# Kernel optimization log

Hardware: AMD Instinct MI355X
Metric: run time of the kernel (lower is better)

The kernel has to match this reference:

```python
import jax, jax.numpy as jnp
import numpy as np

N = 50000
NEG_SLOPE = 0.2  # PyG GATConv default negative_slope


def _gat_layer(x, src, dst, edge_attr, W, We, a_src, a_dst, a_edge, bias):
    """Single-head PyG GATConv (heads=1, concat=True, add_self_loops=True,
    fill_value='mean' for self-loop edge_attr, dropout inactive / eval mode)."""
    n = x.shape[0]
    # add self loops; self-loop edge_attr = per-feature mean of edge_attr
    loop = jnp.arange(n)
    src2 = jnp.concatenate([src, loop])
    dst2 = jnp.concatenate([dst, loop])
    ea_loop = jnp.broadcast_to(edge_attr.mean(axis=0, keepdims=True), (n, edge_attr.shape[1]))
    ea = jnp.concatenate([edge_attr, ea_loop], axis=0)          # [E', edge_dim]

    h = x @ W                                                    # [N, C_out]
    a_s = h @ a_src                                              # [N]
    a_d = h @ a_dst                                              # [N]
    a_e = (ea @ We) @ a_edge                                     # [E']

    alpha = jax.nn.leaky_relu(a_s[src2] + a_d[dst2] + a_e, NEG_SLOPE)  # [E']
    # segment softmax over incoming edges of each dst node
    amax = jax.ops.segment_max(alpha, dst2, num_segments=n)     # [N]
    ex = jnp.exp(alpha - amax[dst2])                             # [E']
    denom = jax.ops.segment_sum(ex, dst2, num_segments=n)       # [N]
    w = ex / denom[dst2]                                         # [E']

    msg = h[src2] * w[:, None]                                   # [E', C_out]
    out = jax.ops.segment_sum(msg, dst2, num_segments=n) + bias  # [N, C_out]
    return out


def setup_inputs() -> dict:
    key = jax.random.key(0)
    ks = jax.random.split(key, 16)
    E, C_in, C_h, C_out, Ed = 800000, 128, 256, 128, 8
    s = 0.05
    inp = {
        "x": jax.random.normal(ks[0], (N, C_in), dtype=jnp.float32),
        "edge_index": jax.random.randint(ks[1], (2, E), 0, N, dtype=jnp.int32),
        "edge_attr": jax.random.normal(ks[2], (E, Ed), dtype=jnp.float32),
        # layer 1 params
        "W1": jax.random.normal(ks[3], (C_in, C_h), dtype=jnp.float32) * s,
        "We1": jax.random.normal(ks[4], (Ed, C_h), dtype=jnp.float32) * s,
        "as1": jax.random.normal(ks[5], (C_h,), dtype=jnp.float32) * s,
        "ad1": jax.random.normal(ks[6], (C_h,), dtype=jnp.float32) * s,
        "ae1": jax.random.normal(ks[7], (C_h,), dtype=jnp.float32) * s,
        "b1": jnp.zeros((C_h,), dtype=jnp.float32),
        # layer 2 params
        "W2": jax.random.normal(ks[8], (C_h, C_out), dtype=jnp.float32) * s,
        "We2": jax.random.normal(ks[9], (Ed, C_out), dtype=jnp.float32) * s,
        "as2": jax.random.normal(ks[10], (C_out,), dtype=jnp.float32) * s,
        "ad2": jax.random.normal(ks[11], (C_out,), dtype=jnp.float32) * s,
        "ae2": jax.random.normal(ks[12], (C_out,), dtype=jnp.float32) * s,
        "b2": jnp.zeros((C_out,), dtype=jnp.float32),
    }
    return inp


def reference(x, edge_index, edge_attr, W1, We1, as1, ad1, ae1, b1,
              W2, We2, as2, ad2, ae2, b2):
    src, dst = edge_index[0], edge_index[1]
    h = _gat_layer(x, src, dst, edge_attr, W1, We1, as1, ad1, ae1, b1)
    h = jax.nn.relu(h)  # relu between layers, not after last
    out = _gat_layer(h, src, dst, edge_attr, W2, We2, as2, ad2, ae2, b2)
    return out
```

## Files before the change

kernel.cpp:

```cpp
#include <hip/hip_runtime.h>
#include <hip/hip_bf16.h>


#define NEG_SLOPE 0.2f
#define EHB 1024

typedef unsigned short u16;
typedef short short8 __attribute__((ext_vector_type(8)));
typedef float v4f __attribute__((ext_vector_type(4)));
typedef u16 u16x4 __attribute__((ext_vector_type(4)));
typedef u16 u16x8 __attribute__((ext_vector_type(8)));

__device__ __forceinline__ u16 f2bf(float f) {
    unsigned u = __float_as_uint(f);
    return (u16)((u + 0x7fffu + ((u >> 16) & 1u)) >> 16);
}
__device__ __forceinline__ float bf2f(u16 h) {
    return __uint_as_float(((unsigned)h) << 16);
}
__device__ __forceinline__ float bf_lo(int v) { return __uint_as_float(((unsigned)v) << 16); }
__device__ __forceinline__ float bf_hi(int v) { return __uint_as_float(((unsigned)v) & 0xffff0000u); }
__device__ __forceinline__ float lrelu(float x) {
    return x >= 0.f ? x : NEG_SLOPE * x;
}
__device__ __forceinline__ int ld_acq(int* p) {
    return __hip_atomic_load(p, __ATOMIC_ACQUIRE, __HIP_MEMORY_SCOPE_AGENT);
}
__device__ __forceinline__ void st_rel(int* p, int v) {
    __hip_atomic_store(p, v, __ATOMIC_RELEASE, __HIP_MEMORY_SCOPE_AGENT);
}

__global__ __launch_bounds__(256) void pre_fat_kernel(
        const float* __restrict__ ea, const int* __restrict__ dst,
        const float* __restrict__ We1, const float* __restrict__ ae1v,
        const float* __restrict__ We2, const float* __restrict__ ae2v,
        float* __restrict__ mean_acc, int* __restrict__ deg,
        float2* __restrict__ aEe, int E,
        const float* __restrict__ W1, u16* __restrict__ w1thi, u16* __restrict__ w1tlo,
        const float* __restrict__ W2, u16* __restrict__ w2thi, u16* __restrict__ w2tlo,
        float* __restrict__ we_vec1g, float* __restrict__ we_vec2g) {
    int tid = threadIdx.x;
    if (blockIdx.x >= EHB) {
        int t = (blockIdx.x - EHB) * 256 + tid;
        if (t < 128 * 256) {
            int k = t >> 8, m = t & 255;
            float v = W1[t];
            u16 h = f2bf(v);
            w1thi[(size_t)m * 128 + k] = h;
            w1tlo[(size_t)m * 128 + k] = f2bf(v - bf2f(h));
        } else {
            t -= 128 * 256;
            int k = t >> 7, m = t & 127;
            float v = W2[t];
            u16 h = f2bf(v);
            w2thi[(size_t)m * 256 + k] = h;
            w2tlo[(size_t)m * 256 + k] = f2bf(v - bf2f(h));
        }
        return;
    }
    __shared__ float red[8];
    __shared__ float wv[16];
    if (tid < 16) { wv[tid] = 0.f; if (tid < 8) red[tid] = 0.f; }
    __syncthreads();
    {
        float a1 = ae1v[tid];
        int lane = tid & 63;
#pragma unroll
        for (int j = 0; j < 8; ++j) {
            float v = We1[j * 256 + tid] * a1;
#pragma unroll
            for (int o = 32; o; o >>= 1) v += __shfl_down(v, o);
            if (lane == 0) atomicAdd(&wv[j], v);
        }
        if (tid < 128) {
            float a2 = ae2v[tid];
#pragma unroll
            for (int j = 0; j < 8; ++j) {
                float v = We2[j * 128 + tid] * a2;
#pragma unroll
                for (int o = 32; o; o >>= 1) v += __shfl_down(v, o);
                if (lane == 0) atomicAdd(&wv[8 + j], v);
            }
        }
    }
    __syncthreads();
    if (blockIdx.x == 0 && tid < 16) {
        if (tid < 8) we_vec1g[tid] = wv[tid];
        else         we_vec2g[tid - 8] = wv[tid];
    }
    float s[8] = {0.f};
    int stride = EHB * 256;
    for (int e = blockIdx.x * 256 + tid; e < E; e += stride) {
        atomicAdd(&deg[dst[e]], 1);
        const float4 v0 = *(const float4*)&ea[(size_t)e * 8];
        const float4 v1 = *(const float4*)&ea[(size_t)e * 8 + 4];
        s[0] += v0.x; s[1] += v0.y; s[2] += v0.z; s[3] += v0.w;
        s[4] += v1.x; s[5] += v1.y; s[6] += v1.z; s[7] += v1.w;
        float s1 = v0.x * wv[0] + v0.y * wv[1] + v0.z * wv[2] + v0.w * wv[3]
                 + v1.x * wv[4] + v1.y * wv[5] + v1.z * wv[6] + v1.w * wv[7];
        float s2 = v0.x * wv[8] + v0.y * wv[9] + v0.z * wv[10] + v0.w * wv[11]
                 + v1.x * wv[12] + v1.y * wv[13] + v1.z * wv[14] + v1.w * wv[15];
        aEe[e] = make_float2(s1, s2);
    }
#pragma unroll
    for (int j = 0; j < 8; ++j) atomicAdd(&red[j], s[j]);
    __syncthreads();
    if (tid < 8) atomicAdd(&mean_acc[tid], red[tid]);
}

__global__ __launch_bounds__(256) void scan_fused_kernel(
        const int* __restrict__ deg, int* __restrict__ row_start,
        int* __restrict__ cursor, int* __restrict__ partials, int* __restrict__ pprefix,
        int* __restrict__ gcount, int* __restrict__ gflag, int N, int n,
        const float* __restrict__ mean_acc, float Einv,
        const float* __restrict__ we_vec1, const float* __restrict__ we_vec2,
        float* __restrict__ ae_loop) {
    __shared__ int s[256];
    __shared__ int amLast, bprefix;
    int t = threadIdx.x, bid = blockIdx.x;
    int i = bid * 256 + t;
    int v = (i < N) ? deg[i] : 0;
    s[t] = v; __syncthreads();
    for (int off = 1; off < 256; off <<= 1) {
        int u = (t >= off) ? s[t - off] : 0;
        __syncthreads();
        s[t] += u;
        __syncthreads();
    }
    int incl = s[t];
    int total = s[255];
    if (t == 0) {
        partials[bid] = total;
        __threadfence();
        int c = __hip_atomic_fetch_add(gcount, 1, __ATOMIC_ACQ_REL, __HIP_MEMORY_SCOPE_AGENT);
        amLast = (c == (int)gridDim.x - 1);
    }
    __syncthreads();
    if (amLast) {
        int G = gridDim.x;
        int pv = (t < G) ? ld_acq(&partials[t]) : 0;
        __syncthreads();
        s[t] = pv; __syncthreads();
        for (int off = 1; off < 256; off <<= 1) {
            int u = (t >= off) ? s[t - off] : 0;
            __syncthreads();
            s[t] += u;
            __syncthreads();
        }
        if (t < G) pprefix[t] = s[t] - pv;
        if (t == 0) {
            float s1 = 0.f, s2 = 0.f;
#pragma unroll
            for (int j = 0; j < 8; ++j) {
                float m = mean_acc[j] * Einv;
                s1 += m * we_vec1[j];
                s2 += m * we_vec2[j];
            }
            ae_loop[0] = s1; ae_loop[1] = s2;
        }
        __threadfence();
        __syncthreads();
        if (t == 0) st_rel(gflag, 1);
    }
    if (t == 0) {
        while (ld_acq(gflag) == 0) __builtin_amdgcn_s_sleep(2);
        bprefix = ld_acq(&pprefix[bid]);
    }
    __syncthreads();
    int ex = bprefix + incl - v;
    if (i < n) row_start[i] = ex;
    if (i < N) cursor[i] = ex;
}

#define BK 32
#define LDA 40
__global__ __launch_bounds__(256) void gemm1_fill_fat_kernel(
        const float* __restrict__ A32,
        const u16* __restrict__ Bh_g, const u16* __restrict__ Bl_g,
        u16* __restrict__ Cb, int Nrows, int K, int M,
        const float* __restrict__ av, const float* __restrict__ bv,
        float* __restrict__ as_out, float* __restrict__ ad_out, int Gg, int gx,
        const int* __restrict__ src, const int* __restrict__ dst,
        const float2* __restrict__ aEe, int* __restrict__ cursor,
        float4* __restrict__ epack, int E) {
    __shared__ u16 Ah[128 * LDA], Bh[128 * LDA], Bl[128 * LDA];
    int tid = threadIdx.x;
    if ((int)blockIdx.x >= Gg) {
        int e = ((int)blockIdx.x - Gg) * 256 + tid;
        if (e < E) {
            int d = dst[e];
            int idx = atomicAdd(&cursor[d], 1);
            float2 a = aEe[e];
            epack[idx] = make_float4(__int_as_float(src[e]), a.x, a.y, 0.f);
        }
        return;
    }
    int lane = tid & 63;
    int wv = tid >> 6;
    int wm = wv >> 1, wn = wv & 1;
    int l15 = lane & 15, quad = lane >> 4;
    int rb = ((int)blockIdx.x / gx) * 128;
    int cb = ((int)blockIdx.x % gx) * 128;

    v4f acc[4][4];
#pragma unroll
    for (int mi = 0; mi < 4; ++mi)
#pragma unroll
        for (int ni = 0; ni < 4; ++ni) acc[mi][ni] = (v4f){0.f, 0.f, 0.f, 0.f};

    int sr = tid >> 1;
    int sc = (tid & 1) * 16;

    for (int kc = 0; kc < K; kc += BK) {
        int gr = rb + sr;
        u16x8 a0 = {0,0,0,0,0,0,0,0}, a1 = {0,0,0,0,0,0,0,0};
        if (gr < Nrows) {
            const float* pa = A32 + (size_t)gr * K + kc + sc;
            float4 f0 = *(const float4*)pa;
            float4 f1 = *(const float4*)(pa + 4);
            float4 f2 = *(const float4*)(pa + 8);
            float4 f3 = *(const float4*)(pa + 12);
            a0 = (u16x8){f2bf(f0.x), f2bf(f0.y), f2bf(f0.z), f2bf(f0.w),
                         f2bf(f1.x), f2bf(f1.y), f2bf(f1.z), f2bf(f1.w)};
            a1 = (u16x8){f2bf(f2.x), f2bf(f2.y), f2bf(f2.z), f2bf(f2.w),
                         f2bf(f3.x), f2bf(f3.y), f2bf(f3.z), f2bf(f3.w)};
        }
        size_t bb = (size_t)(cb + sr) * K + kc + sc;
        u16x8 b0 = *(const u16x8*)(Bh_g + bb);
        u16x8 b1 = *(const u16x8*)(Bh_g + bb + 8);
        u16x8 b2 = *(const u16x8*)(Bl_g + bb);
        u16x8 b3 = *(const u16x8*)(Bl_g + bb + 8);
        *(u16x8*)&Ah[sr * LDA + sc] = a0;
        *(u16x8*)&Ah[sr * LDA + sc + 8] = a1;
        *(u16x8*)&Bh[sr * LDA + sc] = b0;
        *(u16x8*)&Bh[sr * LDA + sc + 8] = b1;
        *(u16x8*)&Bl[sr * LDA + sc] = b2;
        *(u16x8*)&Bl[sr * LDA + sc + 8] = b3;
        __syncthreads();
        short8 ah[4], bh[4], bl[4];
#pragma unroll
        for (int mi = 0; mi < 4; ++mi)
            ah[mi] = *(const short8*)&Ah[(wm * 64 + mi * 16 + l15) * LDA + quad * 8];
#pragma unroll
        for (int ni = 0; ni < 4; ++ni) {
            int r = (wn * 64 + ni * 16 + l15) * LDA + quad * 8;
            bh[ni] = *(const short8*)&Bh[r];
            bl[ni] = *(const short8*)&Bl[r];
        }
#pragma unroll
        for (int mi = 0; mi < 4; ++mi)
#pragma unroll
            for (int ni = 0; ni < 4; ++ni) {
                acc[mi][ni] = __builtin_amdgcn_mfma_f32_16x16x32_bf16(ah[mi], bh[ni], acc[mi][ni], 0, 0, 0);
                acc[mi][ni] = __builtin_amdgcn_mfma_f32_16x16x32_bf16(ah[mi], bl[ni], acc[mi][ni], 0, 0, 0);
            }
        __syncthreads();
    }
#pragma unroll
    for (int mi = 0; mi < 4; ++mi)
#pragma unroll
        for (int ni = 0; ni < 4; ++ni)
#pragma unroll
            for (int reg = 0; reg < 4; ++reg) {
                int row = rb + wm * 64 + mi * 16 + quad * 4 + reg;
                if (row < Nrows)
                    Cb[(size_t)row * M + cb + wn * 64 + ni * 16 + l15] = f2bf(acc[mi][ni][reg]);
            }
    float sd[4][4] = {}, dd[4][4] = {};
#pragma unroll
    for (int ni = 0; ni < 4; ++ni) {
        int col = cb + wn * 64 + ni * 16 + l15;
        float a = av[col], b = bv[col];
#pragma unroll
        for (int mi = 0; mi < 4; ++mi)
#pragma unroll
            for (int reg = 0; reg < 4; ++reg) {
                sd[mi][reg] += acc[mi][ni][reg] * a;
                dd[mi][reg] += acc[mi][ni][reg] * b;
            }
    }
#pragma unroll
    for (int off = 1; off < 16; off <<= 1)
#pragma unroll
        for (int mi = 0; mi < 4; ++mi)
#pragma unroll
            for (int reg = 0; reg < 4; ++reg) {
                sd[mi][reg] += __shfl_xor(sd[mi][reg], off);
                dd[mi][reg] += __shfl_xor(dd[mi][reg], off);
            }
    if (l15 == 0)
#pragma unroll
        for (int mi = 0; mi < 4; ++mi) {
            int row0 = rb + wm * 64 + mi * 16 + quad * 4;
#pragma unroll
            for (int reg = 0; reg < 4; ++reg)
                if (row0 + reg < Nrows) {
                    atomicAdd(as_out + row0 + reg, sd[mi][reg]);
                    atomicAdd(ad_out + row0 + reg, dd[mi][reg]);
                }
        }
}

__global__ __launch_bounds__(256) void gemm_mfma_kernel(
        const u16* __restrict__ A_g,
        const u16* __restrict__ Bh_g, const u16* __restrict__ Bl_g,
        u16* __restrict__ Cb, int Nrows, int K, int M,
        const float* __restrict__ av, const float* __restrict__ bv,
        float* __restrict__ as_out, float* __restrict__ ad_out) {
    __shared__ u16 Ah[128 * LDA], Bh[128 * LDA], Bl[128 * LDA];
    int tid = threadIdx.x;
    int lane = tid & 63;
    int wv = tid >> 6;
    int wm = wv >> 1, wn = wv & 1;
    int l15 = lane & 15, quad = lane >> 4;
    int rb = blockIdx.y * 128;
    int cb = blockIdx.x * 128;

    v4f acc[4][4];
#pragma unroll
    for (int mi = 0; mi < 4; ++mi)
#pragma unroll
        for (int ni = 0; ni < 4; ++ni) acc[mi][ni] = (v4f){0.f, 0.f, 0.f, 0.f};

    int sr = tid >> 1;
    int sc = (tid & 1) * 16;

    for (int kc = 0; kc < K; kc += BK) {
        int gr = rb + sr;
        u16x8 a0 = {0,0,0,0,0,0,0,0}, a1 = {0,0,0,0,0,0,0,0};
        if (gr < Nrows) {
            size_t ba = (size_t)gr * K + kc + sc;
            a0 = *(const u16x8*)(A_g + ba);
            a1 = *(const u16x8*)(A_g + ba + 8);
        }
        size_t bb = (size_t)(cb + sr) * K + kc + sc;
        u16x8 b0 = *(const u16x8*)(Bh_g + bb);
        u16x8 b1 = *(const u16x8*)(Bh_g + bb + 8);
        u16x8 b2 = *(const u16x8*)(Bl_g + bb);
        u16x8 b3 = *(const u16x8*)(Bl_g + bb + 8);
        *(u16x8*)&Ah[sr * LDA + sc] = a0;
        *(u16x8*)&Ah[sr * LDA + sc + 8] = a1;
        *(u16x8*)&Bh[sr * LDA + sc] = b0;
        *(u16x8*)&Bh[sr * LDA + sc + 8] = b1;
        *(u16x8*)&Bl[sr * LDA + sc] = b2;
        *(u16x8*)&Bl[sr * LDA + sc + 8] = b3;
        __syncthreads();
        short8 ah[4], bh[4], bl[4];
#pragma unroll
        for (int mi = 0; mi < 4; ++mi)
            ah[mi] = *(const short8*)&Ah[(wm * 64 + mi * 16 + l15) * LDA + quad * 8];
#pragma unroll
        for (int ni = 0; ni < 4; ++ni) {
            int r = (wn * 64 + ni * 16 + l15) * LDA + quad * 8;
            bh[ni] = *(const short8*)&Bh[r];
            bl[ni] = *(const short8*)&Bl[r];
        }
#pragma unroll
        for (int mi = 0; mi < 4; ++mi)
#pragma unroll
            for (int ni = 0; ni < 4; ++ni) {
                acc[mi][ni] = __builtin_amdgcn_mfma_f32_16x16x32_bf16(ah[mi], bh[ni], acc[mi][ni], 0, 0, 0);
                acc[mi][ni] = __builtin_amdgcn_mfma_f32_16x16x32_bf16(ah[mi], bl[ni], acc[mi][ni], 0, 0, 0);
            }
        __syncthreads();
    }
#pragma unroll
    for (int mi = 0; mi < 4; ++mi)
#pragma unroll
        for (int ni = 0; ni < 4; ++ni)
#pragma unroll
            for (int reg = 0; reg < 4; ++reg) {
                int row = rb + wm * 64 + mi * 16 + quad * 4 + reg;
                if (row < Nrows)
                    Cb[(size_t)row * M + cb + wn * 64 + ni * 16 + l15] = f2bf(acc[mi][ni][reg]);
            }
    float sd[4][4] = {}, dd[4][4] = {};
#pragma unroll
    for (int ni = 0; ni < 4; ++ni) {
        int col = cb + wn * 64 + ni * 16 + l15;
        float a = av[col], b = bv[col];
#pragma unroll
        for (int mi = 0; mi < 4; ++mi)
#pragma unroll
            for (int reg = 0; reg < 4; ++reg) {
                sd[mi][reg] += acc[mi][ni][reg] * a;
                dd[mi][reg] += acc[mi][ni][reg] * b;
            }
    }
#pragma unroll
    for (int off = 1; off < 16; off <<= 1)
#pragma unroll
        for (int mi = 0; mi < 4; ++mi)
#pragma unroll
            for (int reg = 0; reg < 4; ++reg) {
                sd[mi][reg] += __shfl_xor(sd[mi][reg], off);
                dd[mi][reg] += __shfl_xor(dd[mi][reg], off);
            }
    if (l15 == 0)
#pragma unroll
        for (int mi = 0; mi < 4; ++mi) {
            int row0 = rb + wm * 64 + mi * 16 + quad * 4;
#pragma unroll
            for (int reg = 0; reg < 4; ++reg)
                if (row0 + reg < Nrows) {
                    atomicAdd(as_out + row0 + reg, sd[mi][reg]);
                    atomicAdd(ad_out + row0 + reg, dd[mi][reg]);
                }
        }
}

__global__ __launch_bounds__(256) void agg1_kernel(const int* __restrict__ row_start,
                                                   const float4* __restrict__ epack,
                                                   const float* __restrict__ asv,
                                                   const float* __restrict__ adv,
                                                   const float* __restrict__ ae_loop,
                                                   const u16* __restrict__ Hb,
                                                   u16* __restrict__ ohi,
                                                   const float* __restrict__ bias, int N) {
    __shared__ float2 xch[4][64];
    int lane = threadIdx.x & 63;
    int wvi = threadIdx.x >> 6;
    int node = blockIdx.x * 4 + wvi;
    if (node >= N) return;
    int st = row_start[node], en = row_start[node + 1];
    float ad = adv[node];
    float aloop = lrelu(asv[node] + ad + ae_loop[0]);
    float m = aloop, sum = 1.f;
    float acc0, acc1, acc2, acc3;
    {
        int2 hv = *(const int2*)(Hb + (size_t)node * 256 + lane * 4);
        acc0 = bf_lo(hv.x); acc1 = bf_hi(hv.x);
        acc2 = bf_lo(hv.y); acc3 = bf_hi(hv.y);
    }
    for (int base = st; base < en; base += 64) {
        int i = base + lane;
        float al = -3.0e38f; int sreg = 0;
        if (i < en) {
            float4 ep = epack[i];
            sreg = __float_as_int(ep.x);
            al = lrelu(asv[sreg] + ad + ep.y);
        }
        float cm = al;
#pragma unroll
        for (int o = 1; o < 64; o <<= 1) cm = fmaxf(cm, __shfl_xor(cm, o));
        if (cm > m) {
            float sc = __expf(m - cm);
            acc0 *= sc; acc1 *= sc; acc2 *= sc; acc3 *= sc;
            sum *= sc; m = cm;
        }
        float w = (i < en) ? __expf(al - m) : 0.f;
        float wsum = w;
#pragma unroll
        for (int o = 1; o < 64; o <<= 1) wsum += __shfl_xor(wsum, o);
        sum += wsum;
        xch[wvi][lane] = make_float2(w, __int_as_float(sreg));
        int cnt = min(64, en - base);
        int j = 0;
        for (; j + 4 <= cnt; j += 4) {
            float2 e0 = xch[wvi][j], e1 = xch[wvi][j + 1];
            float2 e2 = xch[wvi][j + 2], e3 = xch[wvi][j + 3];
            int2 h0 = *(const int2*)(Hb + (size_t)__float_as_int(e0.y) * 256 + lane * 4);
            int2 h1 = *(const int2*)(Hb + (size_t)__float_as_int(e1.y) * 256 + lane * 4);
            int2 h2 = *(const int2*)(Hb + (size_t)__float_as_int(e2.y) * 256 + lane * 4);
            int2 h3 = *(const int2*)(Hb + (size_t)__float_as_int(e3.y) * 256 + lane * 4);
            acc0 += e0.x * bf_lo(h0.x) + e1.x * bf_lo(h1.x) + e2.x * bf_lo(h2.x) + e3.x * bf_lo(h3.x);
            acc1 += e0.x * bf_hi(h0.x) + e1.x * bf_hi(h1.x) + e2.x * bf_hi(h2.x) + e3.x * bf_hi(h3.x);
            acc2 += e0.x * bf_lo(h0.y) + e1.x * bf_lo(h1.y) + e2.x * bf_lo(h2.y) + e3.x * bf_lo(h3.y);
            acc3 += e0.x * bf_hi(h0.y) + e1.x * bf_hi(h1.y) + e2.x * bf_hi(h2.y) + e3.x * bf_hi(h3.y);
        }
        for (; j < cnt; ++j) {
            float2 e0 = xch[wvi][j];
            int2 h0 = *(const int2*)(Hb + (size_t)__float_as_int(e0.y) * 256 + lane * 4);
            acc0 += e0.x * bf_lo(h0.x); acc1 += e0.x * bf_hi(h0.x);
            acc2 += e0.x * bf_lo(h0.y); acc3 += e0.x * bf_hi(h0.y);
        }
    }
    float inv = 1.f / sum;
    const float4 bvv = *(const float4*)(bias + lane * 4);
    float t0 = acc0 * inv + bvv.x, t1 = acc1 * inv + bvv.y;
    float t2 = acc2 * inv + bvv.z, t3 = acc3 * inv + bvv.w;
    t0 = t0 > 0.f ? t0 : 0.f; t1 = t1 > 0.f ? t1 : 0.f;
    t2 = t2 > 0.f ? t2 : 0.f; t3 = t3 > 0.f ? t3 : 0.f;
    u16x4 h;
    h.x = f2bf(t0); h.y = f2bf(t1); h.z = f2bf(t2); h.w = f2bf(t3);
    *(u16x4*)(ohi + (size_t)node * 256 + lane * 4) = h;
}

__global__ __launch_bounds__(256) void agg2_kernel(const int* __restrict__ row_start,
                                                   const float4* __restrict__ epack,
                                                   const float* __restrict__ asv,
                                                   const float* __restrict__ adv,
                                                   const float* __restrict__ ae_loop,
                                                   const u16* __restrict__ Hb,
                                                   float* __restrict__ out,
                                                   const float* __restrict__ bias, int N) {
    __shared__ float2 xch[4][64];
    int lane = threadIdx.x & 63;
    int wvi = threadIdx.x >> 6;
    int node = blockIdx.x * 4 + wvi;
    if (node >= N) return;
    int st = row_start[node], en = row_start[node + 1];
    float ad = adv[node];
    float aloop = lrelu(asv[node] + ad + ae_loop[1]);
    float m = aloop, sum = 1.f;
    float acc0, acc1;
    {
        int hv = *(const int*)(Hb + (size_t)node * 128 + lane * 2);
        acc0 = bf_lo(hv); acc1 = bf_hi(hv);
    }
    for (int base = st; base < en; base += 64) {
        int i = base + lane;
        float al = -3.0e38f; int sreg = 0;
        if (i < en) {
            float4 ep = epack[i];
            sreg = __float_as_int(ep.x);
            al = lrelu(asv[sreg] + ad + ep.z);
        }
        float cm = al;
#pragma unroll
        for (int o = 1; o < 64; o <<= 1) cm = fmaxf(cm, __shfl_xor(cm, o));
        if (cm > m) {
            float sc = __expf(m - cm);
            acc0 *= sc; acc1 *= sc;
            sum *= sc; m = cm;
        }
        float w = (i < en) ? __expf(al - m) : 0.f;
        float wsum = w;
#pragma unroll
        for (int o = 1; o < 64; o <<= 1) wsum += __shfl_xor(wsum, o);
        sum += wsum;
        xch[wvi][lane] = make_float2(w, __int_as_float(sreg));
        int cnt = min(64, en - base);
        int j = 0;
        for (; j + 4 <= cnt; j += 4) {
            float2 e0 = xch[wvi][j], e1 = xch[wvi][j + 1];
            float2 e2 = xch[wvi][j + 2], e3 = xch[wvi][j + 3];
            int h0 = *(const int*)(Hb + (size_t)__float_as_int(e0.y) * 128 + lane * 2);
            int h1 = *(const int*)(Hb + (size_t)__float_as_int(e1.y) * 128 + lane * 2);
            int h2 = *(const int*)(Hb + (size_t)__float_as_int(e2.y) * 128 + lane * 2);
            int h3 = *(const int*)(Hb + (size_t)__float_as_int(e3.y) * 128 + lane * 2);
            acc0 += e0.x * bf_lo(h0) + e1.x * bf_lo(h1) + e2.x * bf_lo(h2) + e3.x * bf_lo(h3);
            acc1 += e0.x * bf_hi(h0) + e1.x * bf_hi(h1) + e2.x * bf_hi(h2) + e3.x * bf_hi(h3);
        }
        for (; j < cnt; ++j) {
            float2 e0 = xch[wvi][j];
            int h0 = *(const int*)(Hb + (size_t)__float_as_int(e0.y) * 128 + lane * 2);
            acc0 += e0.x * bf_lo(h0); acc1 += e0.x * bf_hi(h0);
        }
    }
    float inv = 1.f / sum;
    size_t o = (size_t)node * 128 + lane * 2;
    out[o]     = acc0 * inv + bias[lane * 2];
    out[o + 1] = acc1 * inv + bias[lane * 2 + 1];
}

extern "C" void kernel_launch(void* const* d_in, const int* in_sizes, int n_in,
                              void* d_out, int out_size, void* d_ws, size_t ws_size,
                              hipStream_t stream) {
    const int Cin = 128, Ch = 256, Co = 128;
    const int N = in_sizes[0] / Cin;
    const int E = in_sizes[1] / 2;

    const float* x   = (const float*)d_in[0];
    const int*   src = (const int*)d_in[1];
    const int*   dst = src + E;
    const float* ea  = (const float*)d_in[2];
    const float* W1  = (const float*)d_in[3];
    const float* We1 = (const float*)d_in[4];
    const float* as1 = (const float*)d_in[5];
    const float* ad1 = (const float*)d_in[6];
    const float* ae1 = (const float*)d_in[7];
    const float* b1  = (const float*)d_in[8];
    const float* W2  = (const float*)d_in[9];
    const float* We2 = (const float*)d_in[10];
    const float* as2 = (const float*)d_in[11];
    const float* ad2 = (const float*)d_in[12];
    const float* ae2 = (const float*)d_in[13];
    const float* b2  = (const float*)d_in[14];
    float* out = (float*)d_out;

    float* ws = (float*)d_ws;
    size_t off = 0;
    u16* h1b = (u16*)(ws + off); off += (size_t)N * Ch / 2;
    u16* g1b = (u16*)(ws + off); off += (size_t)N * Ch / 2;
    float4* epack = (float4*)(ws + off); off += (size_t)E * 4;
    float2* aEe   = (float2*)(ws + off); off += (size_t)E * 2;
    int* row_start = (int*)(ws + off); off += (size_t)N + 1;
    int* cursor    = (int*)(ws + off); off += (size_t)N;
    int* partials  = (int*)(ws + off); off += 256;
    int* pprefix   = (int*)(ws + off); off += 256;
    u16* w1thi = (u16*)(ws + off); off += (size_t)Cin * Ch / 2;
    u16* w1tlo = (u16*)(ws + off); off += (size_t)Cin * Ch / 2;
    u16* w2thi = (u16*)(ws + off); off += (size_t)Ch * Co / 2;
    u16* w2tlo = (u16*)(ws + off); off += (size_t)Ch * Co / 2;
    int*   deg  = (int*)(ws + off); off += (size_t)N + 1;
    float* asv1 = ws + off; off += (size_t)N;
    float* adv1 = ws + off; off += (size_t)N;
    float* asv2 = ws + off; off += (size_t)N;
    float* adv2 = ws + off; off += (size_t)N;
    float* misc = ws + off; off += 32;
    float* mean_acc = misc;
    float* we_vec1  = misc + 8;
    float* we_vec2  = misc + 16;
    float* ae_loop  = misc + 24;
    int* gcount = (int*)(ws + off); off += 1;
    int* gflag  = (int*)(ws + off); off += 1;

    const int n1 = N + 1;
    const int nscan = (n1 + 255) / 256;

    hipMemsetAsync(deg, 0, ((size_t)5 * N + 35) * sizeof(float), stream);

    pre_fat_kernel<<<EHB + 256, 256, 0, stream>>>(
        ea, dst, We1, ae1, We2, ae2, mean_acc, deg, aEe, E,
        W1, w1thi, w1tlo, W2, w2thi, w2tlo, we_vec1, we_vec2);

    scan_fused_kernel<<<nscan, 256, 0, stream>>>(
        deg, row_start, cursor, partials, pprefix, gcount, gflag, N, n1,
        mean_acc, 1.0f / (float)E, we_vec1, we_vec2, ae_loop);

    {
        int gx = Ch / 128;
        int Gg = gx * ((N + 127) / 128);
        int Fb = (E + 255) / 256;
        gemm1_fill_fat_kernel<<<Gg + Fb, 256, 0, stream>>>(
            x, w1thi, w1tlo, h1b, N, Cin, Ch, as1, ad1, asv1, adv1, Gg, gx,
            src, dst, aEe, cursor, epack, E);
    }
    agg1_kernel<<<(N + 3) / 4, 256, 0, stream>>>(row_start, epack, asv1, adv1, ae_loop,
                                                 h1b, g1b, b1, N);

    u16* h2b = h1b;
    {
        dim3 grid(Co / 128, (N + 127) / 128);
        gemm_mfma_kernel<<<grid, 256, 0, stream>>>(g1b, w2thi, w2tlo, h2b, N, Ch, Co,
                                                   as2, ad2, asv2, adv2);
    }
    agg2_kernel<<<(N + 3) / 4, 256, 0, stream>>>(row_start, epack, asv2, adv2, ae_loop,
                                                 h2b, out, b2, N);
}
```

Measured before the change: 397.9 us.

## Fuse CSR edge fill into scan kernel and drop aEe intermediate buffer

```diff
diff --git a/kernel.cpp b/kernel.cpp
--- a/kernel.cpp
+++ b/kernel.cpp
@@ -29,16 +29,15 @@
 __device__ __forceinline__ void st_rel(int* p, int v) {
     __hip_atomic_store(p, v, __ATOMIC_RELEASE, __HIP_MEMORY_SCOPE_AGENT);
 }
+__device__ __forceinline__ float ld_f_agent(const float* p) {
+    return __hip_atomic_load(p, __ATOMIC_RELAXED, __HIP_MEMORY_SCOPE_AGENT);
+}
 
 __global__ __launch_bounds__(256) void pre_fat_kernel(
         const float* __restrict__ ea, const int* __restrict__ dst,
-        const float* __restrict__ We1, const float* __restrict__ ae1v,
-        const float* __restrict__ We2, const float* __restrict__ ae2v,
-        float* __restrict__ mean_acc, int* __restrict__ deg,
-        float2* __restrict__ aEe, int E,
+        float* __restrict__ mean_acc, int* __restrict__ deg, int E,
         const float* __restrict__ W1, u16* __restrict__ w1thi, u16* __restrict__ w1tlo,
-        const float* __restrict__ W2, u16* __restrict__ w2thi, u16* __restrict__ w2tlo,
-        float* __restrict__ we_vec1g, float* __restrict__ we_vec2g) {
+        const float* __restrict__ W2, u16* __restrict__ w2thi, u16* __restrict__ w2tlo) {
     int tid = threadIdx.x;
     if (blockIdx.x >= EHB) {
         int t = (blockIdx.x - EHB) * 256 + tid;
@@ -59,35 +58,8 @@
         return;
     }
     __shared__ float red[8];
-    __shared__ float wv[16];
-    if (tid < 16) { wv[tid] = 0.f; if (tid < 8) red[tid] = 0.f; }
+    if (tid < 8) red[tid] = 0.f;
     __syncthreads();
-    {
-        float a1 = ae1v[tid];
-        int lane = tid & 63;
-#pragma unroll
-        for (int j = 0; j < 8; ++j) {
-            float v = We1[j * 256 + tid] * a1;
-#pragma unroll
-            for (int o = 32; o; o >>= 1) v += __shfl_down(v, o);
-            if (lane == 0) atomicAdd(&wv[j], v);
-        }
-        if (tid < 128) {
-            float a2 = ae2v[tid];
-#pragma unroll
-            for (int j = 0; j < 8; ++j) {
-                float v = We2[j * 128 + tid] * a2;
-#pragma unroll
-                for (int o = 32; o; o >>= 1) v += __shfl_down(v, o);
-                if (lane == 0) atomicAdd(&wv[8 + j], v);
-            }
-        }
-    }
-    __syncthreads();
-    if (blockIdx.x == 0 && tid < 16) {
-        if (tid < 8) we_vec1g[tid] = wv[tid];
-        else         we_vec2g[tid - 8] = wv[tid];
-    }
     float s[8] = {0.f};
     int stride = EHB * 256;
     for (int e = blockIdx.x * 256 + tid; e < E; e += stride) {
@@ -96,11 +68,6 @@
         const float4 v1 = *(const float4*)&ea[(size_t)e * 8 + 4];
         s[0] += v0.x; s[1] += v0.y; s[2] += v0.z; s[3] += v0.w;
         s[4] += v1.x; s[5] += v1.y; s[6] += v1.z; s[7] += v1.w;
-        float s1 = v0.x * wv[0] + v0.y * wv[1] + v0.z * wv[2] + v0.w * wv[3]
-                 + v1.x * wv[4] + v1.y * wv[5] + v1.z * wv[6] + v1.w * wv[7];
-        float s2 = v0.x * wv[8] + v0.y * wv[9] + v0.z * wv[10] + v0.w * wv[11]
-                 + v1.x * wv[12] + v1.y * wv[13] + v1.z * wv[14] + v1.w * wv[15];
-        aEe[e] = make_float2(s1, s2);
     }
 #pragma unroll
     for (int j = 0; j < 8; ++j) atomicAdd(&red[j], s[j]);
@@ -108,99 +75,141 @@
     if (tid < 8) atomicAdd(&mean_acc[tid], red[tid]);
 }
 
-__global__ __launch_bounds__(256) void scan_fused_kernel(
+__global__ __launch_bounds__(256) void scanfill_kernel(
         const int* __restrict__ deg, int* __restrict__ row_start,
         int* __restrict__ cursor, int* __restrict__ partials, int* __restrict__ pprefix,
-        int* __restrict__ gcount, int* __restrict__ gflag, int N, int n,
+        int* __restrict__ gcount, int* __restrict__ gflag1,
+        int* __restrict__ gdone, int* __restrict__ gflag2,
+        int N, int n, int SCB,
         const float* __restrict__ mean_acc, float Einv,
-        const float* __restrict__ we_vec1, const float* __restrict__ we_vec2,
-        float* __restrict__ ae_loop) {
+        const float* __restrict__ We1, const float* __restrict__ ae1v,
+        const float* __restrict__ We2, const float* __restrict__ ae2v,
+        float* __restrict__ we_vec_g, float* __restrict__ ae_loop,
+        const int* __restrict__ src, const int* __restrict__ dst,
+        const float* __restrict__ ea, float4* __restrict__ epack, int E) {
     __shared__ int s[256];
-    __shared__ int amLast, bprefix;
+    __shared__ float wv[16];
+    __shared__ int amLast, bpre_sh;
     int t = threadIdx.x, bid = blockIdx.x;
-    int i = bid * 256 + t;
-    int v = (i < N) ? deg[i] : 0;
-    s[t] = v; __syncthreads();
-    for (int off = 1; off < 256; off <<= 1) {
-        int u = (t >= off) ? s[t - off] : 0;
-        __syncthreads();
-        s[t] += u;
-        __syncthreads();
-    }
-    int incl = s[t];
-    int total = s[255];
-    if (t == 0) {
-        partials[bid] = total;
-        __threadfence();
-        int c = __hip_atomic_fetch_add(gcount, 1, __ATOMIC_ACQ_REL, __HIP_MEMORY_SCOPE_AGENT);
-        amLast = (c == (int)gridDim.x - 1);
-    }
-    __syncthreads();
-    if (amLast) {
-        int G = gridDim.x;
-        int pv = (t < G) ? ld_acq(&partials[t]) : 0;
-        __syncthreads();
-        s[t] = pv; __syncthreads();
+    if (t < 16) wv[t] = 0.f;
+
+    if (bid < SCB) {
+        int i = bid * 256 + t;
+        int v = (i < N) ? deg[i] : 0;
+        s[t] = v; __syncthreads();
         for (int off = 1; off < 256; off <<= 1) {
             int u = (t >= off) ? s[t - off] : 0;
             __syncthreads();
             s[t] += u;
             __syncthreads();
         }
-        if (t < G) pprefix[t] = s[t] - pv;
+        int incl = s[t];
         if (t == 0) {
-            float s1 = 0.f, s2 = 0.f;
-#pragma unroll
-            for (int j = 0; j < 8; ++j) {
-                float m = mean_acc[j] * Einv;
-                s1 += m * we_vec1[j];
-                s2 += m * we_vec2[j];
-            }
-            ae_loop[0] = s1; ae_loop[1] = s2;
-        }
+            partials[bid] = s[255];
+            __threadfence();
+            int c = __hip_atomic_fetch_add(gcount, 1, __ATOMIC_ACQ_REL, __HIP_MEMORY_SCOPE_AGENT);
+            amLast = (c == SCB - 1);
+        }
+        __syncthreads();
+        if (amLast) {
+            int pv = (t < SCB) ? ld_acq(&partials[t]) : 0;
+            __syncthreads();
+            s[t] = pv; __syncthreads();
+            for (int off = 1; off < 256; off <<= 1) {
+                int u = (t >= off) ? s[t - off] : 0;
+                __syncthreads();
+                s[t] += u;
+                __syncthreads();
+            }
+            if (t < SCB) pprefix[t] = s[t] - pv;
+            {
+                int lane = t & 63;
+                float a1 = ae1v[t];
+#pragma unroll
+                for (int j = 0; j < 8; ++j) {
+                    float v2 = We1[j * 256 + t] * a1;
+#pragma unroll
+                    for (int o = 32; o; o >>= 1) v2 += __shfl_down(v2, o);
+                    if (lane == 0) atomicAdd(&wv[j], v2);
+                }
+                if (t < 128) {
+                    float a2 = ae2v[t];
+#pragma unroll
+                    for (int j = 0; j < 8; ++j) {
+                        float v2 = We2[j * 128 + t] * a2;
+#pragma unroll
+                        for (int o = 32; o; o >>= 1) v2 += __shfl_down(v2, o);
+                        if (lane == 0) atomicAdd(&wv[8 + j], v2);
+                    }
+                }
+            }
+            __syncthreads();
+            if (t < 16) we_vec_g[t] = wv[t];
+            if (t == 0) {
+                float s1 = 0.f, s2 = 0.f;
+#pragma unroll
+                for (int j = 0; j < 8; ++j) {
+                    float m = mean_acc[j] * Einv;
+                    s1 += m * wv[j];
+                    s2 += m * wv[8 + j];
+                }
+                ae_loop[0] = s1; ae_loop[1] = s2;
+            }
+            __threadfence();
+            __syncthreads();
+            if (t == 0) st_rel(gflag1, 1);
+        }
+        if (t == 0) {
+            while (ld_acq(gflag1) == 0) __builtin_amdgcn_s_sleep(2);
+            bpre_sh = ld_acq(&pprefix[bid]);
+        }
+        __syncthreads();
+        int ex = bpre_sh + incl - v;
+        if (i < n) row_start[i] = ex;
+        if (i < N) cursor[i] = ex;
         __threadfence();
         __syncthreads();
-        if (t == 0) st_rel(gflag, 1);
+        if (t == 0) {
+            int c2 = __hip_atomic_fetch_add(gdone, 1, __ATOMIC_ACQ_REL, __HIP_MEMORY_SCOPE_AGENT);
+            if (c2 == SCB - 1) st_rel(gflag2, 1);
+        }
     }
     if (t == 0) {
-        while (ld_acq(gflag) == 0) __builtin_amdgcn_s_sleep(2);
-        bprefix = ld_acq(&pprefix[bid]);
+        while (ld_acq(gflag2) == 0) __builtin_amdgcn_s_sleep(2);
     }
     __syncthreads();
-    int ex = bprefix + incl - v;
-    if (i < n) row_start[i] = ex;
-    if (i < N) cursor[i] = ex;
+    if (t < 16) wv[t] = ld_f_agent(&we_vec_g[t]);
+    __syncthreads();
+    int e = bid * 256 + t;
+    if (e < E) {
+        int d = dst[e];
+        int idx = atomicAdd(&cursor[d], 1);
+        const float4 v0 = *(const float4*)&ea[(size_t)e * 8];
+        const float4 v1 = *(const float4*)&ea[(size_t)e * 8 + 4];
+        float s1 = v0.x * wv[0] + v0.y * wv[1] + v0.z * wv[2] + v0.w * wv[3]
+                 + v1.x * wv[4] + v1.y * wv[5] + v1.z * wv[6] + v1.w * wv[7];
+        float s2 = v0.x * wv[8] + v0.y * wv[9] + v0.z * wv[10] + v0.w * wv[11]
+                 + v1.x * wv[12] + v1.y * wv[13] + v1.z * wv[14] + v1.w * wv[15];
+        epack[idx] = make_float4(__int_as_float(src[e]), s1, s2, 0.f);
+    }
 }
 
 #define BK 32
 #define LDA 40
-__global__ __launch_bounds__(256) void gemm1_fill_fat_kernel(
+__global__ __launch_bounds__(256) void gemm1_mfma_kernel(
         const float* __restrict__ A32,
         const u16* __restrict__ Bh_g, const u16* __restrict__ Bl_g,
         u16* __restrict__ Cb, int Nrows, int K, int M,
         const float* __restrict__ av, const float* __restrict__ bv,
-        float* __restrict__ as_out, float* __restrict__ ad_out, int Gg, int gx,
-        const int* __restrict__ src, const int* __restrict__ dst,
-        const float2* __restrict__ aEe, int* __restrict__ cursor,
-        float4* __restrict__ epack, int E) {
+        float* __restrict__ as_out, float* __restrict__ ad_out) {
     __shared__ u16 Ah[128 * LDA], Bh[128 * LDA], Bl[128 * LDA];
     int tid = threadIdx.x;
-    if ((int)blockIdx.x >= Gg) {
-        int e = ((int)blockIdx.x - Gg) * 256 + tid;
-        if (e < E) {
-            int d = dst[e];
-            int idx = atomicAdd(&cursor[d], 1);
-            float2 a = aEe[e];
-            epack[idx] = make_float4(__int_as_float(src[e]), a.x, a.y, 0.f);
-        }
-        return;
-    }
     int lane = tid & 63;
     int wv = tid >> 6;
     int wm = wv >> 1, wn = wv & 1;
     int l15 = lane & 15, quad = lane >> 4;
-    int rb = ((int)blockIdx.x / gx) * 128;
-    int cb = ((int)blockIdx.x % gx) * 128;
+    int rb = blockIdx.y * 128;
+    int cb = blockIdx.x * 128;
 
     v4f acc[4][4];
 #pragma unroll
@@ -584,7 +593,6 @@
     u16* h1b = (u16*)(ws + off); off += (size_t)N * Ch / 2;
     u16* g1b = (u16*)(ws + off); off += (size_t)N * Ch / 2;
     float4* epack = (float4*)(ws + off); off += (size_t)E * 4;
-    float2* aEe   = (float2*)(ws + off); off += (size_t)E * 2;
     int* row_start = (int*)(ws + off); off += (size_t)N + 1;
     int* cursor    = (int*)(ws + off); off += (size_t)N;
     int* partials  = (int*)(ws + off); off += 256;
@@ -600,32 +608,32 @@
     float* adv2 = ws + off; off += (size_t)N;
     float* misc = ws + off; off += 32;
     float* mean_acc = misc;
-    float* we_vec1  = misc + 8;
-    float* we_vec2  = misc + 16;
+    float* we_vec_g = misc + 8;
     float* ae_loop  = misc + 24;
     int* gcount = (int*)(ws + off); off += 1;
-    int* gflag  = (int*)(ws + off); off += 1;
+    int* gflag1 = (int*)(ws + off); off += 1;
+    int* gdone  = (int*)(ws + off); off += 1;
+    int* gflag2 = (int*)(ws + off); off += 1;
 
     const int n1 = N + 1;
-    const int nscan = (n1 + 255) / 256;
-
-    hipMemsetAsync(deg, 0, ((size_t)5 * N + 35) * sizeof(float), stream);
+    const int SCB = (n1 + 255) / 256;
+    const int FB  = (E + 255) / 256;
+
+    hipMemsetAsync(deg, 0, ((size_t)5 * N + 37) * sizeof(float), stream);
 
     pre_fat_kernel<<<EHB + 256, 256, 0, stream>>>(
-        ea, dst, We1, ae1, We2, ae2, mean_acc, deg, aEe, E,
-        W1, w1thi, w1tlo, W2, w2thi, w2tlo, we_vec1, we_vec2);
-
-    scan_fused_kernel<<<nscan, 256, 0, stream>>>(
-        deg, row_start, cursor, partials, pprefix, gcount, gflag, N, n1,
-        mean_acc, 1.0f / (float)E, we_vec1, we_vec2, ae_loop);
+        ea, dst, mean_acc, deg, E, W1, w1thi, w1tlo, W2, w2thi, w2tlo);
+
+    scanfill_kernel<<<FB, 256, 0, stream>>>(
+        deg, row_start, cursor, partials, pprefix, gcount, gflag1, gdone, gflag2,
+        N, n1, SCB, mean_acc, 1.0f / (float)E,
+        We1, ae1, We2, ae2, we_vec_g, ae_loop,
+        src, dst, ea, epack, E);
 
     {
-        int gx = Ch / 128;
-        int Gg = gx * ((N + 127) / 128);
-        int Fb = (E + 255) / 256;
-        gemm1_fill_fat_kernel<<<Gg + Fb, 256, 0, stream>>>(
-            x, w1thi, w1tlo, h1b, N, Cin, Ch, as1, ad1, asv1, adv1, Gg, gx,
-            src, dst, aEe, cursor, epack, E);
+        dim3 grid(Ch / 128, (N + 127) / 128);
+        gemm1_mfma_kernel<<<grid, 256, 0, stream>>>(x, w1thi, w1tlo, h1b, N, Cin, Ch,
+                                                    as1, ad1, asv1, adv1);
     }
     agg1_kernel<<<(N + 3) / 4, 256, 0, stream>>>(row_start, epack, asv1, adv1, ae_loop,
                                                  h1b, g1b, b1, N);
```

After: 788.2 us. 98.1% more time.
